# Kernel tuning notes

Hardware: AMD Instinct MI355X
Metric: run time of the kernel (lower is better)

The kernel has to match this reference:

```python
import jax, jax.numpy as jnp
import numpy as np

N_HEADS = 16

def setup_inputs() -> dict:
    key = jax.random.key(0)
    ks = jax.random.split(key, 9)
    B, L, D = 4, 2048, 1024
    s = D ** -0.5
    return {
        "x": jax.random.normal(ks[0], (B, L, D), dtype=jnp.float32),
        "Wq": jax.random.normal(ks[1], (D, D), dtype=jnp.float32) * s,
        "bq": jax.random.normal(ks[2], (D,), dtype=jnp.float32) * 0.02,
        "Wk": jax.random.normal(ks[3], (D, D), dtype=jnp.float32) * s,
        "bk": jax.random.normal(ks[4], (D,), dtype=jnp.float32) * 0.02,
        "Wv": jax.random.normal(ks[5], (D, D), dtype=jnp.float32) * s,
        "bv": jax.random.normal(ks[6], (D,), dtype=jnp.float32) * 0.02,
        "Wo": jax.random.normal(ks[7], (D, D), dtype=jnp.float32) * s,
        "bo": jax.random.normal(ks[8], (D,), dtype=jnp.float32) * 0.02,
    }

def reference(x, Wq, bq, Wk, bk, Wv, bv, Wo, bo):
    B, L, D = x.shape
    H = N_HEADS
    hd = D // H
    scale = hd ** -0.5
    # torch Linear: y = x @ W.T + b
    q = (x @ Wq.T + bq).reshape(B, L, H, hd)
    k = (x @ Wk.T + bk).reshape(B, L, H, hd)
    v = (x @ Wv.T + bv).reshape(B, L, H, hd)
    # scores [B,H,L,L]
    qk = jnp.einsum('bqhd,bkhd->bhqk', q, k) * scale
    causal = jnp.tril(jnp.ones((L, L), dtype=bool))
    qk = jnp.where(causal[None, None, :, :], qk, -jnp.inf)
    attn = jax.nn.softmax(qk, axis=-1)
    out = jnp.einsum('bhqk,bkhd->bqhd', attn, v).reshape(B, L, D)
    return out @ Wo.T + bo
```

## Files before the change

### kernel.cpp

```cpp
#include <hip/hip_runtime.h>
#include <hip/hip_bf16.h>
#include <math.h>

#define Bsz 4
#define Lsz 2048
#define Dsz 1024
#define Hn 16
#define HDsz 64
#define NQT 16

typedef __attribute__((ext_vector_type(8))) short short8;
typedef __attribute__((ext_vector_type(4))) float floatx4;
typedef unsigned short ushort_t;

__device__ __forceinline__ void load_lds_16B(const void* g, void* l) {
    __builtin_amdgcn_global_load_lds(
        (const __attribute__((address_space(1))) unsigned int*)g,
        (__attribute__((address_space(3))) unsigned int*)l, 16, 0, 0);
}

__device__ inline void cvt_store(float* p, size_t i, float v) { p[i] = v; }
__device__ inline void cvt_store(__hip_bfloat16* p, size_t i, float v) {
    p[i] = __float2bfloat16(v);
}

__device__ inline ushort_t f2bf_raw(float f) {
    __hip_bfloat16 b = __float2bfloat16(f);
    return *reinterpret_cast<ushort_t*>(&b);
}

__device__ inline float bf2f_raw(ushort_t u) {
    union { unsigned int i; float f; } c;
    c.i = ((unsigned int)u) << 16;
    return c.f;
}

__device__ __forceinline__ float fast_exp2(float x) {
#if __has_builtin(__builtin_amdgcn_exp2f)
    return __builtin_amdgcn_exp2f(x);
#else
    return exp2f(x);
#endif
}

__device__ __forceinline__ unsigned pk_bf16_rhu(float p0, float p1) {
    return __builtin_amdgcn_perm(__builtin_bit_cast(unsigned, p1) + 0x8000u,
                                 __builtin_bit_cast(unsigned, p0) + 0x8000u,
                                 0x07060302u);
}

__global__ __launch_bounds__(256) void f2b(const float* __restrict__ in,
                                           __hip_bfloat16* __restrict__ out,
                                           int n) {
    int i = (blockIdx.x * 256 + threadIdx.x) * 4;
    if (i >= n) return;
    float4 v = *(const float4*)(in + i);
    out[i + 0] = __float2bfloat16(v.x);
    out[i + 1] = __float2bfloat16(v.y);
    out[i + 2] = __float2bfloat16(v.z);
    out[i + 3] = __float2bfloat16(v.w);
}

__global__ __launch_bounds__(256) void f2b4(const float* __restrict__ w0,
                                            const float* __restrict__ w1,
                                            const float* __restrict__ w2,
                                            const float* __restrict__ w3,
                                            __hip_bfloat16* __restrict__ out) {
    int bid = blockIdx.x;
    int sel = bid >> 10;
    const float* in = sel == 0 ? w0 : (sel == 1 ? w1 : (sel == 2 ? w2 : w3));
    size_t off = (size_t)(bid & 1023) * 1024 + threadIdx.x * 4;
    float4 v = *(const float4*)(in + off);
    __hip_bfloat16* o = out + (size_t)sel * (1024 * 1024) + off;
    o[0] = __float2bfloat16(v.x);
    o[1] = __float2bfloat16(v.y);
    o[2] = __float2bfloat16(v.z);
    o[3] = __float2bfloat16(v.w);
}

template <typename TO, bool QKV>
__global__ __launch_bounds__(256) void gemm_bt_mfma(
    const ushort_t* __restrict__ A, const ushort_t* __restrict__ W,
    const float* __restrict__ b0, const float* __restrict__ b1,
    const float* __restrict__ b2, TO* __restrict__ C, int M, int N, int K) {
    __shared__ ushort_t As[128 * 32];
    __shared__ ushort_t Bs[128 * 32];

    const int t = threadIdx.x;
    const int wave = t >> 6, lane = t & 63;

    const int nby = M >> 7;
    const int nwg = (N >> 7) * nby;
    const int bid = blockIdx.x;
    const int wg = (bid & 7) * (nwg >> 3) + (bid >> 3);
    const int m0 = (wg % nby) * 128, n0 = (wg / nby) * 128;

    const int wm = (wave & 1) * 64, wn = (wave >> 1) * 64;
    const int lmod = lane & 15, quad = lane >> 4;

    floatx4 acc[4][4] = {};

    for (int k0 = 0; k0 < K; k0 += 32) {
#pragma unroll
        for (int p = 0; p < 2; p++) {
            int chunk = t + p * 256;
            int r = chunk >> 2;
            int c8 = (chunk & 3) * 8;
            load_lds_16B(A + (size_t)(m0 + r) * K + k0 + c8, &As[chunk * 8]);
            load_lds_16B(W + (size_t)(n0 + r) * K + k0 + c8, &Bs[chunk * 8]);
        }
        __syncthreads();

        short8 af[4], bf_[4];
#pragma unroll
        for (int i = 0; i < 4; i++) {
            af[i] = *(const short8*)&As[(wm + i * 16 + lmod) * 32 + quad * 8];
            bf_[i] = *(const short8*)&Bs[(wn + i * 16 + lmod) * 32 + quad * 8];
        }
#pragma unroll
        for (int i = 0; i < 4; i++)
#pragma unroll
            for (int j = 0; j < 4; j++)
                acc[i][j] = __builtin_amdgcn_mfma_f32_16x16x32_bf16(
                    af[i], bf_[j], acc[i][j], 0, 0, 0);
        __syncthreads();
    }

    const int sec = n0 >> 10;
    const float* bp = QKV ? (sec == 0 ? b0 : (sec == 1 ? b1 : b2)) : b0;
    TO* Cb = QKV ? (C + (size_t)sec * M * 1024) : C;
    const int Nout = QKV ? 1024 : N;
    const float sc = (QKV && sec == 0) ? 0.1803368801111204f : 1.0f;

#pragma unroll
    for (int i = 0; i < 4; i++) {
        int gm = m0 + wm + i * 16 + quad * 4;
#pragma unroll
        for (int j = 0; j < 4; j++) {
            int gn = n0 + wn + j * 16 + lmod;
            int cn = QKV ? (gn & 1023) : gn;
            float b = bp[cn];
#pragma unroll
            for (int r = 0; r < 4; r++)
                cvt_store(Cb, (size_t)(gm + r) * Nout + cn,
                          (acc[i][j][r] + b) * sc);
        }
    }
}

__global__ __launch_bounds__(256) void attn_mfma(
    const ushort_t* __restrict__ q, const ushort_t* __restrict__ k,
    const ushort_t* __restrict__ v, ushort_t* __restrict__ Opart,
    float* __restrict__ lpart) {
    __shared__ ushort_t Ks[64 * 64];
    __shared__ ushort_t Vts[64 * 64];
    __shared__ ushort_t Ps[4][32 * 64];

    const int t = threadIdx.x;
    const int wave = t >> 6, lane = t & 63;
    const int lmod = lane & 15, quad = lane >> 4;

    const int bid = blockIdx.x;
    const int j = bid >> 3;
    const int bx = j & 15;
    const int p = bx & 7, s = bx >> 3;
    const int bh = (bid & 7) + ((j >> 4) << 3);
    const int b = bh >> 4, h = bh & 15;
    const size_t base = ((size_t)b * Lsz) * Dsz + h * HDsz;

    const int vrp = t & 31, vcg = t >> 5;
    ushort_t* Pw = (ushort_t*)Ps[wave];
    const int lm7 = lmod & 7;

#pragma unroll 1
    for (int seg = 0; seg < 2; seg++) {
        const int qtile = seg == 0 ? (NQT - 1 - p) : p;
        const int q0 = qtile * 128;
        const int Th = qtile + 1;
        const int kt0 = s * Th, kt1 = kt0 + Th;

        short8 aq[2][2];
#pragma unroll
        for (int g = 0; g < 2; g++) {
            const ushort_t* qp = q + base +
                                 (size_t)(q0 + wave * 32 + g * 16 + lmod) * Dsz +
                                 quad * 8;
            aq[g][0] = *(const short8*)(qp);
            aq[g][1] = *(const short8*)(qp + 32);
        }

        floatx4 Oacc[2][4] = {};
        float lsum[2] = {0.f, 0.f};

        for (int kt = kt0; kt < kt1; kt++) {
            __syncthreads();

#pragma unroll
            for (int pp = 0; pp < 2; pp++) {
                int slot = t + pp * 256;
                int row = slot >> 3, c8 = slot & 7;
                int gc8 = c8 ^ (row & 7);
                load_lds_16B(k + base + (size_t)(kt * 64 + row) * Dsz + gc8 * 8,
                             &Ks[slot * 8]);
            }
            {
                const ushort_t* v0p =
                    v + base + (size_t)(kt * 64 + 2 * vrp) * Dsz + vcg * 8;
                uint4 v0 = *(const uint4*)v0p;
                uint4 v1 = *(const uint4*)(v0p + Dsz);
                unsigned vv0[4] = {v0.x, v0.y, v0.z, v0.w};
                unsigned vv1[4] = {v1.x, v1.y, v1.z, v1.w};
                const int kk = 2 * vrp;
                const int kc8 = kk >> 3, klo = kk & 7;
#pragma unroll
                for (int jj = 0; jj < 4; jj++) {
                    int d0 = vcg * 8 + 2 * jj;
                    unsigned lo =
                        __builtin_amdgcn_perm(vv1[jj], vv0[jj], 0x05040100u);
                    unsigned hi =
                        __builtin_amdgcn_perm(vv1[jj], vv0[jj], 0x07060302u);
                    *(unsigned*)&Vts[d0 * 64 + (kc8 ^ (d0 & 7)) * 8 + klo] = lo;
                    int d1 = d0 + 1;
                    *(unsigned*)&Vts[d1 * 64 + (kc8 ^ (d1 & 7)) * 8 + klo] = hi;
                }
            }
            __syncthreads();

            floatx4 St[2][4] = {};
#pragma unroll
            for (int nt = 0; nt < 4; nt++) {
                int key = nt * 16 + lmod;
#pragma unroll
                for (int ks = 0; ks < 2; ks++) {
                    int sc8 = (ks * 4 + quad) ^ (key & 7);
                    short8 kf = *(const short8*)&Ks[(key * 8 + sc8) * 8];
#pragma unroll
                    for (int g = 0; g < 2; g++)
                        St[g][nt] = __builtin_amdgcn_mfma_f32_16x16x32_bf16(
                            kf, aq[g][ks], St[g][nt], 0, 0, 0);
                }
            }

            const bool need_mask = (kt >= 2 * qtile);
#pragma unroll
            for (int g = 0; g < 2; g++) {
                int qg = q0 + wave * 32 + g * 16 + lmod;
#pragma unroll
                for (int nt = 0; nt < 4; nt++) {
                    int k0g = kt * 64 + nt * 16 + quad * 4;
                    float p0 = fast_exp2(St[g][nt][0]);
                    float p1 = fast_exp2(St[g][nt][1]);
                    float p2 = fast_exp2(St[g][nt][2]);
                    float p3 = fast_exp2(St[g][nt][3]);
                    if (need_mask) {
                        if (k0g + 0 > qg) p0 = 0.f;
                        if (k0g + 1 > qg) p1 = 0.f;
                        if (k0g + 2 > qg) p2 = 0.f;
                        if (k0g + 3 > qg) p3 = 0.f;
                    }
                    lsum[g] += ((p0 + p1) + (p2 + p3));
                    uint2 w;
                    w.x = pk_bf16_rhu(p0, p1);
                    w.y = pk_bf16_rhu(p2, p3);
                    int c8 = nt * 2 + (quad >> 1);
                    int sc8 = c8 ^ lm7;
                    *(uint2*)&Pw[((g * 16 + lmod) * 8 + sc8) * 8 +
                                 (quad & 1) * 4] = w;
                }
            }

            short8 ap[2][2];
#pragma unroll
            for (int g = 0; g < 2; g++)
#pragma unroll
                for (int ks = 0; ks < 2; ks++) {
                    int sc8 = (ks * 4 + quad) ^ lm7;
                    ap[g][ks] =
                        *(const short8*)&Pw[((g * 16 + lmod) * 8 + sc8) * 8];
                }
#pragma unroll
            for (int on = 0; on < 4; on++) {
                int d = on * 16 + lmod;
#pragma unroll
                for (int ks = 0; ks < 2; ks++) {
                    int sc8 = (ks * 4 + quad) ^ (d & 7);
                    short8 bv = *(const short8*)&Vts[(d * 8 + sc8) * 8];
#pragma unroll
                    for (int g = 0; g < 2; g++)
                        Oacc[g][on] = __builtin_amdgcn_mfma_f32_16x16x32_bf16(
                            ap[g][ks], bv, Oacc[g][on], 0, 0, 0);
                }
            }
        }

#pragma unroll
        for (int g = 0; g < 2; g++) {
            lsum[g] += __shfl_xor(lsum[g], 16);
            lsum[g] += __shfl_xor(lsum[g], 32);
        }

        const size_t rec = ((size_t)bh * NQT + qtile) * 2 + s;
        ushort_t* Orec = Opart + rec * (128 * 64);
        float* lrec = lpart + rec * 128;
#pragma unroll
        for (int g = 0; g < 2; g++) {
            if (quad == 0) lrec[wave * 32 + g * 16 + lmod] = lsum[g];
#pragma unroll
            for (int r = 0; r < 4; r++) {
                int row = wave * 32 + g * 16 + quad * 4 + r;
#pragma unroll
                for (int on = 0; on < 4; on++) {
                    int d = on * 16 + lmod;
                    Orec[row * 64 + d] = f2bf_raw(Oacc[g][on][r]);
                }
            }
        }
    }
}

__global__ __launch_bounds__(256) void attn_combine(
    const ushort_t* __restrict__ Opart, const float* __restrict__ lpart,
    ushort_t* __restrict__ ao) {
    int gidx = blockIdx.x * 256 + threadIdx.x;
    int rowglob = gidx >> 3;
    int c8 = (gidx & 7) * 8;
    int bh = rowglob >> 11;
    int r11 = rowglob & 2047;
    int qtile = r11 >> 7, row = r11 & 127;

    size_t rec0 = ((size_t)bh * NQT + qtile) * 2;
    const ushort_t* O0 = Opart + (rec0 + 0) * (128 * 64) + row * 64 + c8;
    const ushort_t* O1 = Opart + (rec0 + 1) * (128 * 64) + row * 64 + c8;
    float l = lpart[(rec0 + 0) * 128 + row] + lpart[(rec0 + 1) * 128 + row];
    float inv = 1.0f / l;

    short8 a = *(const short8*)O0;
    short8 bvec = *(const short8*)O1;
    short8 o;
#pragma unroll
    for (int j = 0; j < 8; j++) {
        float vv = (bf2f_raw((ushort_t)a[j]) + bf2f_raw((ushort_t)bvec[j])) * inv;
        o[j] = (short)f2bf_raw(vv);
    }
    int b = bh >> 4, h = bh & 15;
    int qg = qtile * 128 + row;
    *(short8*)&ao[((size_t)(b * Lsz + qg)) * Dsz + h * HDsz + c8] = o;
}

extern "C" void kernel_launch(void* const* d_in, const int* in_sizes, int n_in,
                              void* d_out, int out_size, void* d_ws,
                              size_t ws_size, hipStream_t stream) {
    const size_t elems = (size_t)Bsz * Lsz * Dsz;
    const size_t welem = (size_t)Dsz * Dsz;
    const size_t nrec = (size_t)Bsz * Hn * NQT * 2;
    const size_t opart_e = nrec * 128 * 64;
    const size_t need = (5 * elems + 4 * welem + opart_e) * 2 + nrec * 128 * 4;
    if (ws_size < need) return;

    const float* x = (const float*)d_in[0];
    const float* Wq = (const float*)d_in[1];
    const float* bq = (const float*)d_in[2];
    const float* Wk = (const float*)d_in[3];
    const float* bk = (const float*)d_in[4];
    const float* Wv = (const float*)d_in[5];
    const float* bv = (const float*)d_in[6];
    const float* Wo = (const float*)d_in[7];
    const float* bo = (const float*)d_in[8];
    float* out = (float*)d_out;

    __hip_bfloat16* xb = (__hip_bfloat16*)d_ws;
    __hip_bfloat16* q = xb + elems;
    __hip_bfloat16* k = q + elems;
    __hip_bfloat16* v = k + elems;
    __hip_bfloat16* ao = v + elems;
    __hip_bfloat16* Wqb = ao + elems;
    __hip_bfloat16* Wkb = Wqb + welem;
    __hip_bfloat16* Wvb = Wkb + welem;
    __hip_bfloat16* Wob = Wvb + welem;
    ushort_t* Opart = (ushort_t*)(Wob + welem);
    float* lpart = (float*)(Opart + opart_e);

    const int M = Bsz * Lsz, N = Dsz, K = Dsz;

    f2b<<<(int)(elems / 4 + 255) / 256, 256, 0, stream>>>(x, xb, (int)elems);
    f2b4<<<4096, 256, 0, stream>>>(Wq, Wk, Wv, Wo, Wqb);

    gemm_bt_mfma<__hip_bfloat16, true><<<3 * N / 128 * (M / 128), 256, 0,
                                         stream>>>(
        (const ushort_t*)xb, (const ushort_t*)Wqb, bq, bk, bv, q, M, 3 * N, K);

    attn_mfma<<<16 * Bsz * Hn, 256, 0, stream>>>(
        (const ushort_t*)q, (const ushort_t*)k, (const ushort_t*)v, Opart,
        lpart);

    attn_combine<<<(int)(elems / 8 / 256), 256, 0, stream>>>(Opart, lpart,
                                                             (ushort_t*)ao);

    gemm_bt_mfma<float, false><<<N / 128 * (M / 128), 256, 0, stream>>>(
        (const ushort_t*)ao, (const ushort_t*)Wob, bo, bo, bo, out, M, N, K);
}
```

Before: 293.7 us.

## Add 256x256 double-buffered swizzled MFMA GEMM for QKV projection

Adds a new 512-thread GEMM kernel with 256x256 tiles, K-step 64, double-buffered LDS with XOR-swizzled layout, and interleaved prefetch/compute phases using setprio, and uses it for the fused QKV projection. The aim is higher arithmetic intensity per workgroup and overlap of global-to-LDS loads with MFMA work. The old 128-tile kernel's block ordering is also changed to N-major traversal for the output projection. The larger tile needs 128KB of LDS and a large accumulator set, which may limit occupancy, and the small tile count may leave CUs underfilled.

New measurement: 282.3 us. 3.9% less time.

```diff
diff --git a/kernel.cpp b/kernel.cpp
--- a/kernel.cpp
+++ b/kernel.cpp
@@ -79,6 +79,152 @@
 }
 
 template <typename TO, bool QKV>
+__global__ __launch_bounds__(512, 2) void gemm_bt_256(
+    const ushort_t* __restrict__ A, const ushort_t* __restrict__ W,
+    const float* __restrict__ b0, const float* __restrict__ b1,
+    const float* __restrict__ b2, TO* __restrict__ C, int M, int N, int K) {
+    __shared__ ushort_t As[2][256 * 64];
+    __shared__ ushort_t Bs[2][256 * 64];
+
+    const int t = threadIdx.x;
+    const int wave = t >> 6, lane = t & 63;
+    const int lmod = lane & 15, quad = lane >> 4;
+    const int wm = wave >> 2, wn = wave & 3;
+
+    const int nbn = N >> 8;
+    const int nwg = nbn * (M >> 8);
+    const int bid = blockIdx.x;
+    const int wg = (bid & 7) * (nwg >> 3) + (bid >> 3);
+    const int n0 = (wg % nbn) * 256, m0 = (wg / nbn) * 256;
+
+    floatx4 acc[2][2][4][2] = {};
+    short8 Af[4][2], Bf[2][2];
+
+    const int NT = K >> 6;
+
+    auto stageA = [&](int kt, int bi) {
+        const int kk = kt << 6;
+#pragma unroll
+        for (int p = 0; p < 4; p++) {
+            int slot = t + p * 512;
+            int row = slot >> 3, c8 = slot & 7;
+            int gc8 = c8 ^ (row & 7);
+            load_lds_16B(A + (size_t)(m0 + row) * K + kk + gc8 * 8,
+                         &As[bi][slot * 8]);
+        }
+    };
+    auto stageB = [&](int kt, int bi) {
+        const int kk = kt << 6;
+#pragma unroll
+        for (int p = 0; p < 4; p++) {
+            int slot = t + p * 512;
+            int row = slot >> 3, c8 = slot & 7;
+            int gc8 = c8 ^ (row & 7);
+            load_lds_16B(W + (size_t)(n0 + row) * K + kk + gc8 * 8,
+                         &Bs[bi][slot * 8]);
+        }
+    };
+    auto rdA = [&](int bi, int mh) {
+#pragma unroll
+        for (int mr = 0; mr < 4; mr++) {
+            int row = wm * 128 + mh * 64 + mr * 16 + lmod;
+#pragma unroll
+            for (int ks = 0; ks < 2; ks++) {
+                int sc8 = (ks * 4 + quad) ^ (row & 7);
+                Af[mr][ks] = *(const short8*)&As[bi][row * 64 + sc8 * 8];
+            }
+        }
+    };
+    auto rdB = [&](int bi, int nh) {
+#pragma unroll
+        for (int nr = 0; nr < 2; nr++) {
+            int row = wn * 64 + nh * 32 + nr * 16 + lmod;
+#pragma unroll
+            for (int ks = 0; ks < 2; ks++) {
+                int sc8 = (ks * 4 + quad) ^ (row & 7);
+                Bf[nr][ks] = *(const short8*)&Bs[bi][row * 64 + sc8 * 8];
+            }
+        }
+    };
+    auto domm = [&](int mh, int nh) {
+        __builtin_amdgcn_s_setprio(1);
+#pragma unroll
+        for (int mr = 0; mr < 4; mr++)
+#pragma unroll
+            for (int nr = 0; nr < 2; nr++)
+#pragma unroll
+                for (int ks = 0; ks < 2; ks++)
+                    acc[mh][nh][mr][nr] =
+                        __builtin_amdgcn_mfma_f32_16x16x32_bf16(
+                            Af[mr][ks], Bf[nr][ks], acc[mh][nh][mr][nr], 0, 0,
+                            0);
+        __builtin_amdgcn_s_setprio(0);
+    };
+
+    stageA(0, 0);
+    stageB(0, 0);
+    asm volatile("s_waitcnt vmcnt(0)" ::: "memory");
+    __builtin_amdgcn_s_barrier();
+    asm volatile("" ::: "memory");
+
+#pragma unroll 1
+    for (int T = 0; T < NT; T++) {
+        const int cur = T & 1, nxt = cur ^ 1;
+        const bool pf = (T + 1 < NT);
+        rdA(cur, 0);
+        rdB(cur, 0);
+        if (pf) stageA(T + 1, nxt);
+        __builtin_amdgcn_s_barrier();
+        __builtin_amdgcn_sched_barrier(0);
+        domm(0, 0);
+        __builtin_amdgcn_s_barrier();
+        rdB(cur, 1);
+        if (pf) stageB(T + 1, nxt);
+        __builtin_amdgcn_s_barrier();
+        __builtin_amdgcn_sched_barrier(0);
+        domm(0, 1);
+        __builtin_amdgcn_s_barrier();
+        rdA(cur, 1);
+        __builtin_amdgcn_s_barrier();
+        __builtin_amdgcn_sched_barrier(0);
+        domm(1, 1);
+        __builtin_amdgcn_s_barrier();
+        rdB(cur, 0);
+        __builtin_amdgcn_s_barrier();
+        __builtin_amdgcn_sched_barrier(0);
+        domm(1, 0);
+        asm volatile("s_waitcnt vmcnt(0)" ::: "memory");
+        __builtin_amdgcn_s_barrier();
+        asm volatile("" ::: "memory");
+    }
+
+    const int sec = QKV ? (n0 >> 10) : 0;
+    const float* bp = QKV ? (sec == 0 ? b0 : (sec == 1 ? b1 : b2)) : b0;
+    TO* Cb = QKV ? (C + (size_t)sec * M * 1024) : C;
+    const int Nout = QKV ? 1024 : N;
+    const float sc = (QKV && sec == 0) ? 0.1803368801111204f : 1.0f;
+
+#pragma unroll
+    for (int mh = 0; mh < 2; mh++)
+#pragma unroll
+        for (int mr = 0; mr < 4; mr++) {
+            int gm = m0 + wm * 128 + mh * 64 + mr * 16 + quad * 4;
+#pragma unroll
+            for (int nh = 0; nh < 2; nh++)
+#pragma unroll
+                for (int nr = 0; nr < 2; nr++) {
+                    int gn = n0 + wn * 64 + nh * 32 + nr * 16 + lmod;
+                    int cn = QKV ? (gn & 1023) : gn;
+                    float b = bp[cn];
+#pragma unroll
+                    for (int r = 0; r < 4; r++)
+                        cvt_store(Cb, (size_t)(gm + r) * Nout + cn,
+                                  (acc[mh][nh][mr][nr][r] + b) * sc);
+                }
+        }
+}
+
+template <typename TO, bool QKV>
 __global__ __launch_bounds__(256) void gemm_bt_mfma(
     const ushort_t* __restrict__ A, const ushort_t* __restrict__ W,
     const float* __restrict__ b0, const float* __restrict__ b1,
@@ -89,11 +235,11 @@
     const int t = threadIdx.x;
     const int wave = t >> 6, lane = t & 63;
 
-    const int nby = M >> 7;
-    const int nwg = (N >> 7) * nby;
+    const int nbx = N >> 7;
+    const int nwg = nbx * (M >> 7);
     const int bid = blockIdx.x;
     const int wg = (bid & 7) * (nwg >> 3) + (bid >> 3);
-    const int m0 = (wg % nby) * 128, n0 = (wg / nby) * 128;
+    const int n0 = (wg % nbx) * 128, m0 = (wg / nbx) * 128;
 
     const int wm = (wave & 1) * 64, wn = (wave >> 1) * 64;
     const int lmod = lane & 15, quad = lane >> 4;
@@ -385,8 +531,8 @@
     f2b<<<(int)(elems / 4 + 255) / 256, 256, 0, stream>>>(x, xb, (int)elems);
     f2b4<<<4096, 256, 0, stream>>>(Wq, Wk, Wv, Wo, Wqb);
 
-    gemm_bt_mfma<__hip_bfloat16, true><<<3 * N / 128 * (M / 128), 256, 0,
-                                         stream>>>(
+    gemm_bt_256<__hip_bfloat16, true><<<(3 * N / 256) * (M / 256), 512, 0,
+                                        stream>>>(
         (const ushort_t*)xb, (const ushort_t*)Wqb, bq, bk, bv, q, M, 3 * N, K);
 
     attn_mfma<<<16 * Bsz * Hn, 256, 0, stream>>>(
```
